# Kernel tuning notes

Measured on AMD Instinct MI355X. Metric: run time of the kernel, lower is better.

## Reference

```python
import jax, jax.numpy as jnp
import numpy as np
from jax import lax

B, CIN, COUT, H, W = 16, 128, 256, 56, 56
KH, KW = 3, 3
STRIDE = (1, 1)
PAD = ((1, 1), (1, 1))
DILATION = (1, 1)
GROUPS = 1


def setup_inputs() -> dict:
    key = jax.random.key(0)
    k1, k2, k3 = jax.random.split(key, 3)
    x = jax.random.normal(k1, (B, CIN, H, W), dtype=jnp.float32)
    weight = jax.random.normal(k2, (COUT, CIN // GROUPS, KH, KW), dtype=jnp.float32)
    bias = jax.random.normal(k3, (COUT,), dtype=jnp.float32)
    return {"x": x, "weight": weight, "bias": bias}


def reference(x, weight, bias):
    # Toeplitz matrix-vector product == grouped 2D convolution (cross-correlation)
    # with zero padding, plus per-output-channel bias.
    out = lax.conv_general_dilated(
        x, weight,
        window_strides=STRIDE,
        padding=PAD,
        rhs_dilation=DILATION,
        dimension_numbers=("NCHW", "OIHW", "NCHW"),
        feature_group_count=GROUPS,
    )
    return out + bias[None, :, None, None]
```

## Files before the change

kernel.cpp:

```cpp
#include <hip/hip_runtime.h>
#include <hip/hip_bf16.h>


#define XT_BYTES   15204352u
#define SLACK      8192u
#define WT_OFFSET  (XT_BYTES + SLACK)
#define WT_BYTES   589824u
#define WS_NEED    (WT_OFFSET + WT_BYTES)

typedef __bf16 bf16x8 __attribute__((ext_vector_type(8)));
typedef float  f32x4  __attribute__((ext_vector_type(4)));
typedef unsigned short ushort8v __attribute__((ext_vector_type(8)));

__device__ __forceinline__ unsigned short f2bf(float f) {
  unsigned u = __builtin_bit_cast(unsigned, f);
  u += 0x7fffu + ((u >> 16) & 1u);
  return (unsigned short)(u >> 16);
}

__device__ __forceinline__ void gll16(const void* g, const void* l) {
  __builtin_amdgcn_global_load_lds(
      (const __attribute__((address_space(1))) unsigned int*)g,
      (__attribute__((address_space(3))) unsigned int*)l, 16, 0, 0);
}

__global__ void prep(const float* __restrict__ x, const float* __restrict__ wsrc,
                     unsigned short* __restrict__ xt, unsigned short* __restrict__ wt) {
  int blk = blockIdx.x;
  int t = threadIdx.x;
  if (blk < 896) {
    __shared__ unsigned short tile[128][58];
    int b = blk / 56, h = blk % 56;
    int ci = t >> 1, half = t & 1;
    const float* src = x + ((size_t)(b * 128 + ci)) * 3136 + h * 56 + half * 28;
    #pragma unroll
    for (int q = 0; q < 7; ++q) {
      float4 v = *(const float4*)&src[q * 4];
      int wb = half * 28 + q * 4;
      tile[ci][wb + 0] = f2bf(v.x);
      tile[ci][wb + 1] = f2bf(v.y);
      tile[ci][wb + 2] = f2bf(v.z);
      tile[ci][wb + 3] = f2bf(v.w);
    }
    unsigned short* row = xt + (size_t)b * 475136 + (size_t)(h + 1) * 8192;
    if (t < 128) {
      int slot = t >> 4;
      int px = slot ? 56 + slot : 0;
      uint4 z; z.x = z.y = z.z = z.w = 0u;
      *(uint4*)(row + px * 128 + (t & 15) * 8) = z;
    }
    __syncthreads();
    if (t < 224) {
      int wo = t >> 2, chunk = t & 3;
      unsigned short* dst = row + (size_t)(wo + 1) * 128 + chunk * 32;
      #pragma unroll
      for (int q = 0; q < 4; ++q) {
        ushort8v v;
        #pragma unroll
        for (int j = 0; j < 8; ++j) v[j] = tile[chunk * 32 + q * 8 + j][wo];
        *(ushort8v*)&dst[q * 8] = v;
      }
    }
  } else if (blk < 928) {
    int idx = blk - 896;
    int b = idx >> 1, zr = (idx & 1) ? 57 : 0;
    uint4* dst = (uint4*)(xt + (size_t)b * 475136 + (size_t)zr * 8192);
    uint4 z; z.x = z.y = z.z = z.w = 0u;
    #pragma unroll
    for (int q = 0; q < 4; ++q) dst[t + q * 256] = z;
  } else {
    int k64 = blk - 928;
    int tap = k64 >> 1;
    int ci_base = (k64 & 1) * 64;
    #pragma unroll
    for (int h = 0; h < 2; ++h) {
      int kt = k64 * 2 + h;
      int ci0 = ci_base + h * 32;
      #pragma unroll
      for (int pm = 0; pm < 2; ++pm) {
        #pragma unroll
        for (int q = 0; q < 2; ++q) {
          int n = t + q * 256;
          int r = n >> 2, s = n & 3;
          int kg = s ^ (r & 3);
          int co = pm * 128 + r;
          const float* src = wsrc + (size_t)co * 1152 + (size_t)(ci0 + kg * 8) * 9 + tap;
          ushort8v v;
          #pragma unroll
          for (int j = 0; j < 8; ++j) v[j] = f2bf(src[j * 9]);
          *(ushort8v*)&wt[((size_t)kt * 2 + pm) * 4096 + n * 8] = v;
        }
      }
    }
  }
}


__global__ __launch_bounds__(256, 5) void conv_gemm(
    const unsigned short* __restrict__ xt,
    const char* __restrict__ wt,
    const float* __restrict__ bias,
    float* __restrict__ out) {
  __shared__ __align__(16) char lds[32768];

  int bid = blockIdx.x;
  int sw = (bid & 7) * 112 + (bid >> 3);
  int pm = sw & 1;
  int pn = sw >> 1;
  int bimg = pn / 28;
  int h0 = (pn - bimg * 28) * 2;

  int tid = threadIdx.x;
  int wv = tid >> 6, l = tid & 63;
  int wm = wv >> 1, wn = wv & 1;
  int lm = l & 15, lg = l >> 4;
  int swz = ((lg ^ (lm & 3)) << 4);

  int aoff0 = wm * 4096 + lm * 64 + swz;
  int boff0 = 8192 + wn * 4096 + lm * 64 + swz;

  const char* aB = wt + pm * 8192 + (wv * 64 + l) * 16;
  const unsigned short* bB[2];
  #pragma unroll
  for (int j = 0; j < 2; ++j) {
    int n = wv * 64 + l + j * 256;
    int px = n >> 2;
    int kg = (n & 3) ^ (px & 3);
    bB[j] = xt + ((size_t)((bimg * 58 + h0 + (px >> 6)) * 64 + (px & 63))) * 128 + kg * 8;
  }

  f32x4 acc[4][4];
  #pragma unroll
  for (int m = 0; m < 4; ++m)
    #pragma unroll
    for (int n = 0; n < 4; ++n)
      acc[m][n] = (f32x4){0.f, 0.f, 0.f, 0.f};

  auto stage = [&](int kt, int buf) {
    int tap = kt >> 2;
    int kh = tap >= 6 ? 2 : (tap >= 3 ? 1 : 0);
    int kw = tap - kh * 3;
    int koff = (kh * 64 + kw) * 128 + (kt & 3) * 32;
    const char* sA = aB + kt * 16384;
    char* dA = &lds[buf * 16384 + (wv * 64 + l) * 16];
    char* dB = dA + 8192;
    gll16(sA, dA);
    gll16(sA + 4096, dA + 4096);
    gll16(bB[0] + koff, dB);
    gll16(bB[1] + koff, dB + 4096);
  };

  stage(0, 0);
  __syncthreads();

  for (int kt = 0; kt < 36; ++kt) {
    const char* base = &lds[(kt & 1) * 16384];
    if (kt < 35) stage(kt + 1, (kt + 1) & 1);
    bf16x8 a[4], b[4];
    #pragma unroll
    for (int m = 0; m < 4; ++m) a[m] = *(const bf16x8*)(base + aoff0 + m * 1024);
    #pragma unroll
    for (int n = 0; n < 4; ++n) b[n] = *(const bf16x8*)(base + boff0 + n * 1024);
    #pragma unroll
    for (int m = 0; m < 4; ++m)
      #pragma unroll
      for (int n = 0; n < 4; ++n)
        acc[m][n] = __builtin_amdgcn_mfma_f32_16x16x32_bf16(a[m], b[n], acc[m][n], 0, 0, 0);
    if (kt < 35) __syncthreads();
  }

  #pragma unroll
  for (int m = 0; m < 4; ++m) {
    int co = pm * 128 + wm * 64 + m * 16 + lg * 4;
    f32x4 bb = *(const f32x4*)&bias[co];
    size_t obase = ((size_t)bimg * 256 + co) * 3136;
    #pragma unroll
    for (int n = 0; n < 4; ++n) {
      int px = wn * 64 + n * 16 + lm;
      int w_ = px & 63;
      int h_ = h0 + (px >> 6);
      if (w_ < 56) {
        float* o = out + obase + (size_t)h_ * 56 + w_;
        #pragma unroll
        for (int r = 0; r < 4; ++r)
          o[(size_t)r * 3136] = acc[m][n][r] + bb[r];
      }
    }
  }
}


__global__ void conv_naive(const float* __restrict__ x, const float* __restrict__ w,
                           const float* __restrict__ bias, float* __restrict__ out) {
  int idx = blockIdx.x * 256 + threadIdx.x;
  if (idx >= 16 * 256 * 56 * 56) return;
  int wo = idx % 56; int t = idx / 56;
  int ho = t % 56; t /= 56;
  int co = t % 256; int b = t / 256;
  float acc = bias[co];
  for (int ci = 0; ci < 128; ++ci) {
    const float* xp = x + ((size_t)(b * 128 + ci)) * 3136;
    const float* wp = w + ((size_t)(co * 128 + ci)) * 9;
    for (int kh = 0; kh < 3; ++kh) {
      int hi = ho + kh - 1;
      if (hi < 0 || hi >= 56) continue;
      for (int kw = 0; kw < 3; ++kw) {
        int wi = wo + kw - 1;
        if (wi < 0 || wi >= 56) continue;
        acc += xp[hi * 56 + wi] * wp[kh * 3 + kw];
      }
    }
  }
  out[idx] = acc;
}

extern "C" void kernel_launch(void* const* d_in, const int* in_sizes, int n_in,
                              void* d_out, int out_size, void* d_ws, size_t ws_size,
                              hipStream_t stream) {
  const float* x    = (const float*)d_in[0];
  const float* wgt  = (const float*)d_in[1];
  const float* bias = (const float*)d_in[2];
  float* out = (float*)d_out;

  if (ws_size < (size_t)WS_NEED) {
    conv_naive<<<(16 * 256 * 56 * 56 + 255) / 256, 256, 0, stream>>>(x, wgt, bias, out);
    return;
  }

  unsigned short* xt = (unsigned short*)d_ws;
  unsigned short* wt = (unsigned short*)((char*)d_ws + WT_OFFSET);

  prep<<<946, 256, 0, stream>>>(x, wgt, xt, wt);
  conv_gemm<<<896, 256, 0, stream>>>(xt, (const char*)wt, bias, out);
}
```

Measured before the change: 63.45 us.

## Enlarge GEMM tile to full 256 output channels with triple-buffered LDS pipeline

Each conv_gemm block now computes all 256 output channels for its 128-pixel tile instead of half, so the input tile is loaded once rather than twice. The grid is halved to 448 blocks, and the weight layout and swizzle are changed to match. The double buffer becomes a three-stage LDS ring with explicit vmcnt waits and raw barriers, so loads are issued two steps ahead. The cost is more accumulator registers and 72KB of LDS, which limits occupancy to about 2 blocks per CU, and 448 blocks may underfill the 256 CUs.

```diff
diff --git a/kernel.cpp b/kernel.cpp
--- a/kernel.cpp
+++ b/kernel.cpp
@@ -11,6 +11,9 @@
 typedef __bf16 bf16x8 __attribute__((ext_vector_type(8)));
 typedef float  f32x4  __attribute__((ext_vector_type(4)));
 typedef unsigned short ushort8v __attribute__((ext_vector_type(8)));
+
+#define BAR()   __builtin_amdgcn_s_barrier()
+#define SB0()   __builtin_amdgcn_sched_barrier(0)
 
 __device__ __forceinline__ unsigned short f2bf(float f) {
   unsigned u = __builtin_bit_cast(unsigned, f);
@@ -69,69 +72,69 @@
     #pragma unroll
     for (int q = 0; q < 4; ++q) dst[t + q * 256] = z;
   } else {
-    int k64 = blk - 928;
-    int tap = k64 >> 1;
-    int ci_base = (k64 & 1) * 64;
-    #pragma unroll
-    for (int h = 0; h < 2; ++h) {
-      int kt = k64 * 2 + h;
-      int ci0 = ci_base + h * 32;
+    int base_kt = (blk - 928) * 2;
+    #pragma unroll
+    for (int kk = 0; kk < 2; ++kk) {
+      int kt = base_kt + kk;
+      int tap = kt >> 2, ci0 = (kt & 3) * 32;
       #pragma unroll
-      for (int pm = 0; pm < 2; ++pm) {
+      for (int q = 0; q < 4; ++q) {
+        int n = t + q * 256;
+        int co = n >> 2, p = n & 3;
+        int kg = p ^ ((co >> 1) & 3);
+        const float* src = wsrc + (size_t)co * 1152 + (size_t)(ci0 + kg * 8) * 9 + tap;
+        ushort8v v;
         #pragma unroll
-        for (int q = 0; q < 2; ++q) {
-          int n = t + q * 256;
-          int r = n >> 2, s = n & 3;
-          int kg = s ^ (r & 3);
-          int co = pm * 128 + r;
-          const float* src = wsrc + (size_t)co * 1152 + (size_t)(ci0 + kg * 8) * 9 + tap;
-          ushort8v v;
-          #pragma unroll
-          for (int j = 0; j < 8; ++j) v[j] = f2bf(src[j * 9]);
-          *(ushort8v*)&wt[((size_t)kt * 2 + pm) * 4096 + n * 8] = v;
-        }
-      }
-    }
-  }
-}
-
-
-__global__ __launch_bounds__(256, 5) void conv_gemm(
+        for (int j = 0; j < 8; ++j) v[j] = f2bf(src[j * 9]);
+        *(ushort8v*)&wt[(size_t)kt * 8192 + n * 8] = v;
+      }
+    }
+  }
+}
+
+
+__global__ __launch_bounds__(256, 2) void conv_gemm(
     const unsigned short* __restrict__ xt,
     const char* __restrict__ wt,
     const float* __restrict__ bias,
     float* __restrict__ out) {
-  __shared__ __align__(16) char lds[32768];
+  __shared__ __align__(16) char lds[73728];
 
   int bid = blockIdx.x;
-  int sw = (bid & 7) * 112 + (bid >> 3);
-  int pm = sw & 1;
-  int pn = sw >> 1;
-  int bimg = pn / 28;
-  int h0 = (pn - bimg * 28) * 2;
+  int sw = (bid & 7) * 56 + (bid >> 3);
+  int bimg = sw / 28;
+  int h0 = (sw - bimg * 28) * 2;
 
   int tid = threadIdx.x;
   int wv = tid >> 6, l = tid & 63;
   int wm = wv >> 1, wn = wv & 1;
   int lm = l & 15, lg = l >> 4;
-  int swz = ((lg ^ (lm & 3)) << 4);
-
-  int aoff0 = wm * 4096 + lm * 64 + swz;
-  int boff0 = 8192 + wn * 4096 + lm * 64 + swz;
-
-  const char* aB = wt + pm * 8192 + (wv * 64 + l) * 16;
-  const unsigned short* bB[2];
+
+  int aRd[8], bRd[4];
+  #pragma unroll
+  for (int m = 0; m < 8; ++m) {
+    int row = wm * 128 + m * 16 + lm;
+    aRd[m] = row * 64 + ((lg ^ ((row >> 1) & 3)) << 4);
+  }
+  #pragma unroll
+  for (int n = 0; n < 4; ++n) {
+    int row = wn * 64 + n * 16 + lm;
+    bRd[n] = 16384 + row * 64 + ((lg ^ ((row >> 1) & 3)) << 4);
+  }
+
+  const char* aS = wt + tid * 16;
+  const unsigned short* bS[2];
   #pragma unroll
   for (int j = 0; j < 2; ++j) {
-    int n = wv * 64 + l + j * 256;
-    int px = n >> 2;
-    int kg = (n & 3) ^ (px & 3);
-    bB[j] = xt + ((size_t)((bimg * 58 + h0 + (px >> 6)) * 64 + (px & 63))) * 128 + kg * 8;
-  }
-
-  f32x4 acc[4][4];
-  #pragma unroll
-  for (int m = 0; m < 4; ++m)
+    int n = tid + j * 256;
+    int px = n >> 2, p = n & 3;
+    int kg = p ^ ((px >> 1) & 3);
+    bS[j] = xt + ((size_t)((bimg * 58 + h0 + (px >> 6)) * 64 + (px & 63))) * 128 + kg * 8;
+  }
+
+  f32x4 acc[8][4];
+  #pragma unroll
+  for (int m = 0; m < 8; ++m)
     #pragma unroll
     for (int n = 0; n < 4; ++n)
       acc[m][n] = (f32x4){0.f, 0.f, 0.f, 0.f};
@@ -141,37 +144,44 @@
     int kh = tap >= 6 ? 2 : (tap >= 3 ? 1 : 0);
     int kw = tap - kh * 3;
     int koff = (kh * 64 + kw) * 128 + (kt & 3) * 32;
-    const char* sA = aB + kt * 16384;
-    char* dA = &lds[buf * 16384 + (wv * 64 + l) * 16];
-    char* dB = dA + 8192;
-    gll16(sA, dA);
-    gll16(sA + 4096, dA + 4096);
-    gll16(bB[0] + koff, dB);
-    gll16(bB[1] + koff, dB + 4096);
+    const char* sA = aS + kt * 16384;
+    char* d = &lds[buf * 24576 + tid * 16];
+    #pragma unroll
+    for (int q = 0; q < 4; ++q) gll16(sA + q * 4096, d + q * 4096);
+    char* dB = &lds[buf * 24576 + 16384 + tid * 16];
+    gll16(bS[0] + koff, dB);
+    gll16(bS[1] + koff, dB + 4096);
   };
 
   stage(0, 0);
-  __syncthreads();
-
+  stage(1, 1);
+  asm volatile("s_waitcnt vmcnt(6)" ::: "memory");
+  SB0(); BAR(); SB0();
+
+  int cb = 0;
   for (int kt = 0; kt < 36; ++kt) {
-    const char* base = &lds[(kt & 1) * 16384];
-    if (kt < 35) stage(kt + 1, (kt + 1) & 1);
-    bf16x8 a[4], b[4];
-    #pragma unroll
-    for (int m = 0; m < 4; ++m) a[m] = *(const bf16x8*)(base + aoff0 + m * 1024);
-    #pragma unroll
-    for (int n = 0; n < 4; ++n) b[n] = *(const bf16x8*)(base + boff0 + n * 1024);
-    #pragma unroll
-    for (int m = 0; m < 4; ++m)
+    int nb = cb >= 1 ? cb - 1 : 2;
+    if (kt < 34) stage(kt + 2, nb);
+    const char* base = &lds[cb * 24576];
+    bf16x8 a[8], b[4];
+    #pragma unroll
+    for (int m = 0; m < 8; ++m) a[m] = *(const bf16x8*)(base + aRd[m]);
+    #pragma unroll
+    for (int n = 0; n < 4; ++n) b[n] = *(const bf16x8*)(base + bRd[n]);
+    #pragma unroll
+    for (int m = 0; m < 8; ++m)
       #pragma unroll
       for (int n = 0; n < 4; ++n)
         acc[m][n] = __builtin_amdgcn_mfma_f32_16x16x32_bf16(a[m], b[n], acc[m][n], 0, 0, 0);
-    if (kt < 35) __syncthreads();
-  }
-
-  #pragma unroll
-  for (int m = 0; m < 4; ++m) {
-    int co = pm * 128 + wm * 64 + m * 16 + lg * 4;
+    if (kt < 34)       asm volatile("s_waitcnt vmcnt(6)" ::: "memory");
+    else if (kt == 34) asm volatile("s_waitcnt vmcnt(0)" ::: "memory");
+    SB0(); BAR(); SB0();
+    cb = cb == 2 ? 0 : cb + 1;
+  }
+
+  #pragma unroll
+  for (int m = 0; m < 8; ++m) {
+    int co = wm * 128 + m * 16 + lg * 4;
     f32x4 bb = *(const f32x4*)&bias[co];
     size_t obase = ((size_t)bimg * 256 + co) * 3136;
     #pragma unroll
@@ -231,5 +241,5 @@
   unsigned short* wt = (unsigned short*)((char*)d_ws + WT_OFFSET);
 
   prep<<<946, 256, 0, stream>>>(x, wgt, xt, wt);
-  conv_gemm<<<896, 256, 0, stream>>>(xt, (const char*)wt, bias, out);
-}
+  conv_gemm<<<448, 256, 0, stream>>>(xt, (const char*)wt, bias, out);
+}
```

Measured after the change: 57.88 us. -8.8%, faster.

## Switch conv GEMM to 32x32x16 MFMA and repack input transpose

Applied to the files above, without the earlier changes.

The GEMM kernel now uses 32x32x16 bf16 MFMA tiles instead of 16x16x32, with a new LDS swizzle (XOR on row>>1) that matches the wider fragment reads. The weight and activation prep layouts are changed to fit this swizzle. The prep kernel now handles two rows per block, packs channel pairs into LDS and writes 16-byte rows, which cuts the grid from 946 to 498 blocks. Launch bounds drop from 5 to 3 waves per SIMD to leave room for the 16-wide accumulators, which may lower occupancy.

```diff
diff --git a/kernel.cpp b/kernel.cpp
--- a/kernel.cpp
+++ b/kernel.cpp
@@ -10,6 +10,7 @@
 
 typedef __bf16 bf16x8 __attribute__((ext_vector_type(8)));
 typedef float  f32x4  __attribute__((ext_vector_type(4)));
+typedef float  f32x16 __attribute__((ext_vector_type(16)));
 typedef unsigned short ushort8v __attribute__((ext_vector_type(8)));
 
 __device__ __forceinline__ unsigned short f2bf(float f) {
@@ -28,67 +29,65 @@
                      unsigned short* __restrict__ xt, unsigned short* __restrict__ wt) {
   int blk = blockIdx.x;
   int t = threadIdx.x;
-  if (blk < 896) {
-    __shared__ unsigned short tile[128][58];
-    int b = blk / 56, h = blk % 56;
-    int ci = t >> 1, half = t & 1;
-    const float* src = x + ((size_t)(b * 128 + ci)) * 3136 + h * 56 + half * 28;
+  if (blk < 448) {
+    __shared__ unsigned short tile[2][58][136];
+    int b = blk / 28, hp = blk % 28;
+    int ci2 = t & 63, half = (t >> 6) & 1, hh = t >> 7;
+    int h = hp * 2 + hh;
+    const float* s0 = x + ((size_t)(b * 128 + ci2 * 2)) * 3136 + h * 56 + half * 28;
+    const float* s1 = s0 + 3136;
     #pragma unroll
     for (int q = 0; q < 7; ++q) {
-      float4 v = *(const float4*)&src[q * 4];
-      int wb = half * 28 + q * 4;
-      tile[ci][wb + 0] = f2bf(v.x);
-      tile[ci][wb + 1] = f2bf(v.y);
-      tile[ci][wb + 2] = f2bf(v.z);
-      tile[ci][wb + 3] = f2bf(v.w);
-    }
-    unsigned short* row = xt + (size_t)b * 475136 + (size_t)(h + 1) * 8192;
-    if (t < 128) {
-      int slot = t >> 4;
-      int px = slot ? 56 + slot : 0;
+      float4 v0 = *(const float4*)&s0[q * 4];
+      float4 v1 = *(const float4*)&s1[q * 4];
+      int w = 1 + half * 28 + q * 4;
+      unsigned short* dst = &tile[hh][0][0] + (size_t)w * 136 + ci2 * 2;
+      *(unsigned*)(dst)       = (unsigned)f2bf(v0.x) | ((unsigned)f2bf(v1.x) << 16);
+      *(unsigned*)(dst + 136) = (unsigned)f2bf(v0.y) | ((unsigned)f2bf(v1.y) << 16);
+      *(unsigned*)(dst + 272) = (unsigned)f2bf(v0.z) | ((unsigned)f2bf(v1.z) << 16);
+      *(unsigned*)(dst + 408) = (unsigned)f2bf(v0.w) | ((unsigned)f2bf(v1.w) << 16);
+    }
+    __syncthreads();
+    int s = t & 127, hh2 = t >> 7;
+    int w = s >> 1, part = s & 1;
+    unsigned short* dst = xt + (size_t)b * 475136 +
+                          (size_t)(hp * 2 + hh2 + 1) * 8192 + w * 128 + part * 64;
+    if (w == 0 || w >= 57) {
       uint4 z; z.x = z.y = z.z = z.w = 0u;
-      *(uint4*)(row + px * 128 + (t & 15) * 8) = z;
-    }
-    __syncthreads();
-    if (t < 224) {
-      int wo = t >> 2, chunk = t & 3;
-      unsigned short* dst = row + (size_t)(wo + 1) * 128 + chunk * 32;
-      #pragma unroll
-      for (int q = 0; q < 4; ++q) {
-        ushort8v v;
-        #pragma unroll
-        for (int j = 0; j < 8; ++j) v[j] = tile[chunk * 32 + q * 8 + j][wo];
-        *(ushort8v*)&dst[q * 8] = v;
-      }
-    }
-  } else if (blk < 928) {
-    int idx = blk - 896;
+      #pragma unroll
+      for (int i = 0; i < 8; ++i) *(uint4*)(dst + i * 8) = z;
+    } else {
+      const unsigned short* srcl = &tile[hh2][0][0] + (size_t)w * 136 + part * 64;
+      #pragma unroll
+      for (int i = 0; i < 8; ++i)
+        *(uint4*)(dst + i * 8) = *(const uint4*)(srcl + i * 8);
+    }
+  } else if (blk < 480) {
+    int idx = blk - 448;
     int b = idx >> 1, zr = (idx & 1) ? 57 : 0;
     uint4* dst = (uint4*)(xt + (size_t)b * 475136 + (size_t)zr * 8192);
     uint4 z; z.x = z.y = z.z = z.w = 0u;
     #pragma unroll
     for (int q = 0; q < 4; ++q) dst[t + q * 256] = z;
   } else {
-    int k64 = blk - 928;
-    int tap = k64 >> 1;
-    int ci_base = (k64 & 1) * 64;
-    #pragma unroll
-    for (int h = 0; h < 2; ++h) {
-      int kt = k64 * 2 + h;
-      int ci0 = ci_base + h * 32;
+    int kidx = blk - 480;
+    #pragma unroll
+    for (int kk = 0; kk < 2; ++kk) {
+      int kt = kidx * 2 + kk;
+      int tap = kt >> 2, ci0 = (kt & 3) * 32;
       #pragma unroll
       for (int pm = 0; pm < 2; ++pm) {
         #pragma unroll
         for (int q = 0; q < 2; ++q) {
           int n = t + q * 256;
-          int r = n >> 2, s = n & 3;
-          int kg = s ^ (r & 3);
+          int r = n >> 2, sslot = n & 3;
+          int kg = sslot ^ ((r >> 1) & 3);
           int co = pm * 128 + r;
           const float* src = wsrc + (size_t)co * 1152 + (size_t)(ci0 + kg * 8) * 9 + tap;
           ushort8v v;
           #pragma unroll
           for (int j = 0; j < 8; ++j) v[j] = f2bf(src[j * 9]);
-          *(ushort8v*)&wt[((size_t)kt * 2 + pm) * 4096 + n * 8] = v;
+          *(ushort8v*)&wt[((size_t)kt * 1024 + pm * 512 + n) * 8] = v;
         }
       }
     }
@@ -96,7 +95,7 @@
 }
 
 
-__global__ __launch_bounds__(256, 5) void conv_gemm(
+__global__ __launch_bounds__(256, 3) void conv_gemm(
     const unsigned short* __restrict__ xt,
     const char* __restrict__ wt,
     const float* __restrict__ bias,
@@ -113,41 +112,50 @@
   int tid = threadIdx.x;
   int wv = tid >> 6, l = tid & 63;
   int wm = wv >> 1, wn = wv & 1;
-  int lm = l & 15, lg = l >> 4;
-  int swz = ((lg ^ (lm & 3)) << 4);
-
-  int aoff0 = wm * 4096 + lm * 64 + swz;
-  int boff0 = 8192 + wn * 4096 + lm * 64 + swz;
-
-  const char* aB = wt + pm * 8192 + (wv * 64 + l) * 16;
-  const unsigned short* bB[2];
+  int l31 = l & 31, lg2 = l >> 5;
+  int rx = (l >> 1) & 3;
+
+  int aRd[2][2], bRd[2][2];
+  #pragma unroll
+  for (int mb = 0; mb < 2; ++mb)
+    #pragma unroll
+    for (int k16 = 0; k16 < 2; ++k16) {
+      int row = wm * 64 + mb * 32 + l31;
+      aRd[mb][k16] = row * 64 + (((k16 * 2 + lg2) ^ rx) << 4);
+      int prow = wn * 64 + mb * 32 + l31;
+      bRd[mb][k16] = 8192 + prow * 64 + (((k16 * 2 + lg2) ^ rx) << 4);
+    }
+
+  const char* aS = wt + pm * 8192 + tid * 16;
+  const unsigned short* bS[2];
   #pragma unroll
   for (int j = 0; j < 2; ++j) {
-    int n = wv * 64 + l + j * 256;
-    int px = n >> 2;
-    int kg = (n & 3) ^ (px & 3);
-    bB[j] = xt + ((size_t)((bimg * 58 + h0 + (px >> 6)) * 64 + (px & 63))) * 128 + kg * 8;
-  }
-
-  f32x4 acc[4][4];
-  #pragma unroll
-  for (int m = 0; m < 4; ++m)
-    #pragma unroll
-    for (int n = 0; n < 4; ++n)
-      acc[m][n] = (f32x4){0.f, 0.f, 0.f, 0.f};
+    int n = tid + j * 256;
+    int px = n >> 2, p = n & 3;
+    int kg = p ^ ((px >> 1) & 3);
+    bS[j] = xt + ((size_t)((bimg * 58 + h0 + (px >> 6)) * 64 + (px & 63))) * 128 + kg * 8;
+  }
+
+  f32x16 acc[2][2];
+  #pragma unroll
+  for (int mb = 0; mb < 2; ++mb)
+    #pragma unroll
+    for (int nb = 0; nb < 2; ++nb)
+      #pragma unroll
+      for (int e = 0; e < 16; ++e) acc[mb][nb][e] = 0.f;
 
   auto stage = [&](int kt, int buf) {
     int tap = kt >> 2;
     int kh = tap >= 6 ? 2 : (tap >= 3 ? 1 : 0);
     int kw = tap - kh * 3;
     int koff = (kh * 64 + kw) * 128 + (kt & 3) * 32;
-    const char* sA = aB + kt * 16384;
-    char* dA = &lds[buf * 16384 + (wv * 64 + l) * 16];
-    char* dB = dA + 8192;
+    const char* sA = aS + kt * 16384;
+    char* dA = &lds[buf * 16384 + tid * 16];
+    char* dB = &lds[buf * 16384 + 8192 + tid * 16];
     gll16(sA, dA);
     gll16(sA + 4096, dA + 4096);
-    gll16(bB[0] + koff, dB);
-    gll16(bB[1] + koff, dB + 4096);
+    gll16(bS[0] + koff, dB);
+    gll16(bS[1] + koff, dB + 4096);
   };
 
   stage(0, 0);
@@ -156,37 +164,43 @@
   for (int kt = 0; kt < 36; ++kt) {
     const char* base = &lds[(kt & 1) * 16384];
     if (kt < 35) stage(kt + 1, (kt + 1) & 1);
-    bf16x8 a[4], b[4];
-    #pragma unroll
-    for (int m = 0; m < 4; ++m) a[m] = *(const bf16x8*)(base + aoff0 + m * 1024);
-    #pragma unroll
-    for (int n = 0; n < 4; ++n) b[n] = *(const bf16x8*)(base + boff0 + n * 1024);
-    #pragma unroll
-    for (int m = 0; m < 4; ++m)
-      #pragma unroll
-      for (int n = 0; n < 4; ++n)
-        acc[m][n] = __builtin_amdgcn_mfma_f32_16x16x32_bf16(a[m], b[n], acc[m][n], 0, 0, 0);
+    bf16x8 a[2][2], b[2][2];
+    #pragma unroll
+    for (int mb = 0; mb < 2; ++mb)
+      #pragma unroll
+      for (int k16 = 0; k16 < 2; ++k16) {
+        a[mb][k16] = *(const bf16x8*)(base + aRd[mb][k16]);
+        b[mb][k16] = *(const bf16x8*)(base + bRd[mb][k16]);
+      }
+    #pragma unroll
+    for (int mb = 0; mb < 2; ++mb)
+      #pragma unroll
+      for (int nb = 0; nb < 2; ++nb) {
+        acc[mb][nb] = __builtin_amdgcn_mfma_f32_32x32x16_bf16(a[mb][0], b[nb][0], acc[mb][nb], 0, 0, 0);
+        acc[mb][nb] = __builtin_amdgcn_mfma_f32_32x32x16_bf16(a[mb][1], b[nb][1], acc[mb][nb], 0, 0, 0);
+      }
     if (kt < 35) __syncthreads();
   }
 
   #pragma unroll
-  for (int m = 0; m < 4; ++m) {
-    int co = pm * 128 + wm * 64 + m * 16 + lg * 4;
-    f32x4 bb = *(const f32x4*)&bias[co];
-    size_t obase = ((size_t)bimg * 256 + co) * 3136;
-    #pragma unroll
-    for (int n = 0; n < 4; ++n) {
-      int px = wn * 64 + n * 16 + lm;
+  for (int mb = 0; mb < 2; ++mb)
+    #pragma unroll
+    for (int nb = 0; nb < 2; ++nb) {
+      int px = wn * 64 + nb * 32 + l31;
       int w_ = px & 63;
       int h_ = h0 + (px >> 6);
       if (w_ < 56) {
-        float* o = out + obase + (size_t)h_ * 56 + w_;
         #pragma unroll
-        for (int r = 0; r < 4; ++r)
-          o[(size_t)r * 3136] = acc[m][n][r] + bb[r];
-      }
-    }
-  }
+        for (int q = 0; q < 4; ++q) {
+          int co0 = pm * 128 + wm * 64 + mb * 32 + q * 8 + lg2 * 4;
+          f32x4 bb = *(const f32x4*)&bias[co0];
+          float* o = out + ((size_t)(bimg * 256 + co0)) * 3136 + (size_t)h_ * 56 + w_;
+          #pragma unroll
+          for (int j = 0; j < 4; ++j)
+            o[(size_t)j * 3136] = acc[mb][nb][q * 4 + j] + bb[j];
+        }
+      }
+    }
 }
 
 
@@ -230,6 +244,6 @@
   unsigned short* xt = (unsigned short*)d_ws;
   unsigned short* wt = (unsigned short*)((char*)d_ws + WT_OFFSET);
 
-  prep<<<946, 256, 0, stream>>>(x, wgt, xt, wt);
+  prep<<<498, 256, 0, stream>>>(x, wgt, xt, wt);
   conv_gemm<<<896, 256, 0, stream>>>(xt, (const char*)wt, bias, out);
 }
```

Result: no change. 64.51 us (+1.7%).
